# Kernel optimization log

Hardware: AMD Instinct MI355X
Metric: run time of the kernel (lower is better)

The kernel has to match this reference:

```python
import math
import jax, jax.numpy as jnp
import numpy as np
from jax import lax

L = 16
T = 256
FDIM = 3
N_MIN = 4
N_MAX = 64
INIT_RANGE = 1e-4
# low 32 bits of the products are exact in uint32, and XOR + (% T) with T=256
# only reads the low 8 bits, so uint32 arithmetic matches torch's int64 exactly.
PI = jnp.array([1, 2654435761, 805459861], dtype=jnp.uint32)

def _levels():
    growth = math.exp(math.log(N_MAX / N_MIN) / (L - 1))
    return [math.floor(N_MIN * growth ** l) for l in range(L)]

def setup_inputs() -> dict:
    key = jax.random.key(0)
    kx, kt = jax.random.split(key)
    x = jax.random.uniform(kx, (4, 3, 64, 64, 64), dtype=jnp.float32)
    hash_table = (jax.random.uniform(kt, (L, T, FDIM), dtype=jnp.float32) * 2.0
                  - 1.0) * INIT_RANGE
    return {"x": x, "hash_table": hash_table}

def _forward(x, hash_table):
    b, c, h, w, d = x.shape
    outs = []
    for l, n in enumerate(_levels()):
        kh, kw, kd = h // n, w // n, d // n
        # max_pool3d with kernel==stride, VALID padding (torch default)
        pooled = lax.reduce_window(x * n, -jnp.inf, lax.max,
                                   (1, 1, kh, kw, kd), (1, 1, kh, kw, kd),
                                   'VALID')  # [b, 3, nh, nw, nd]
        g = pooled.astype(jnp.uint32)  # trunc toward zero (values >= 0)
        g = g * PI.reshape(1, 3, 1, 1, 1)
        gh = (g[:, 0] ^ g[:, 1] ^ g[:, 2]) % jnp.uint32(T)  # [b, nh, nw, nd]
        feat = hash_table[l][gh]                 # [b, nh, nw, nd, F] gather
        feat = jnp.transpose(feat, (0, 4, 1, 3, 2))  # [b, F, nh, nd, nw]
        up = jax.image.resize(feat, (b, FDIM, h, w, d), method='trilinear')
        outs.append(up)
    return jnp.concatenate(outs, axis=1)  # [b, L*F, h, w, d]

def reference(x, hash_table):
    return _forward(x, hash_table)
```

## Files before the change

kernel.cpp:

```cpp
#include <hip/hip_runtime.h>
#include <cmath>
#include <cstdint>
#include <cstddef>

using u32 = unsigned int;
typedef float f32x4 __attribute__((ext_vector_type(4)));

__device__ inline void st4(float* p, float a, float b, float c, float d)
{
    f32x4 v; v.x = a; v.y = b; v.z = c; v.w = d;
    *(f32x4*)p = v;
}

constexpr int NH[12] = {4,4,5,6,8,10,12,16,21,21,32,32};

constexpr int OFF_M2  = 0;
constexpr int OFF_M3  = 393216;
constexpr int OFF_M5  = 504348;
constexpr int OFF_M4  = 525084;
constexpr int OFF_M6  = 574236;
constexpr int OFF_M8  = 586236;
constexpr int OFF_M10 = 592380;
constexpr int OFF_M12 = 594972;
constexpr int OFF_M16 = 596472;

constexpr int POFF[12] = {OFF_M16,OFF_M16,OFF_M12,OFF_M10,OFF_M8,OFF_M6,
                          OFF_M5, OFF_M4, OFF_M3, OFF_M3, OFF_M2, OFF_M2};

constexpr float invf_of(int nh){ return (float)(1.0/(64.0/(double)nh)); }
constexpr float INVF[12] = {invf_of(4),invf_of(4),invf_of(5),invf_of(6),
                            invf_of(8),invf_of(10),invf_of(12),invf_of(16),
                            invf_of(21),invf_of(21),invf_of(32),invf_of(32)};

struct HP { int n[16]; };

__device__ inline float lp(float a, float b, float w){ return fmaf(w, b - a, a); }

__global__ __launch_bounds__(256) void k_pool_base(const float* __restrict__ x,
                                                   float* __restrict__ ws)
{
    int tid = blockIdx.x * 256 + threadIdx.x;
    if (tid < 393216) {
        int pd = tid & 31, pw = (tid >> 5) & 31, ph = (tid >> 10) & 31;
        int bc = tid >> 15;
        const float* xp = x + (size_t)bc * 262144 + (ph*2)*4096 + (pw*2)*64 + pd*2;
        float2 v00 = *(const float2*)(xp);
        float2 v01 = *(const float2*)(xp + 64);
        float2 v10 = *(const float2*)(xp + 4096);
        float2 v11 = *(const float2*)(xp + 4160);
        float m = fmaxf(fmaxf(fmaxf(v00.x,v00.y), fmaxf(v01.x,v01.y)),
                        fmaxf(fmaxf(v10.x,v10.y), fmaxf(v11.x,v11.y)));
        ws[OFF_M2 + tid] = m;
    } else if (tid < 504348) {
        int idx = tid - 393216;
        int pd = idx % 21; int t2 = idx / 21;
        int pw = t2 % 21;  int t3 = t2 / 21;
        int ph = t3 % 21;  int bc = t3 / 21;
        const float* xp = x + (size_t)bc * 262144 + (ph*3)*4096 + (pw*3)*64 + pd*3;
        float m = -1.f;
        #pragma unroll
        for (int dh = 0; dh < 3; ++dh)
        #pragma unroll
        for (int dw = 0; dw < 3; ++dw) {
            const float* r = xp + dh*4096 + dw*64;
            m = fmaxf(m, fmaxf(fmaxf(r[0], r[1]), r[2]));
        }
        ws[OFF_M3 + idx] = m;
    } else if (tid < 525084) {
        int idx = tid - 504348;
        int pd = idx % 12; int t2 = idx / 12;
        int pw = t2 % 12;  int t3 = t2 / 12;
        int ph = t3 % 12;  int bc = t3 / 12;
        const float* xp = x + (size_t)bc * 262144 + (ph*5)*4096 + (pw*5)*64 + pd*5;
        float m = -1.f;
        #pragma unroll
        for (int dh = 0; dh < 5; ++dh)
        #pragma unroll
        for (int dw = 0; dw < 5; ++dw) {
            const float* r = xp + dh*4096 + dw*64;
            m = fmaxf(m, fmaxf(fmaxf(fmaxf(r[0],r[1]), fmaxf(r[2],r[3])), r[4]));
        }
        ws[OFF_M5 + idx] = m;
    }
}

__global__ __launch_bounds__(256) void k_pyr(float* __restrict__ ws)
{
    int tid = blockIdx.x * 256 + threadIdx.x;
    if (tid < 49152) {
        int w = tid >> 6, lane = tid & 63;
        int pd = w & 3, pw = (w >> 2) & 3, ph = (w >> 4) & 3, bc = w >> 6;
        const float* m2 = ws + OFF_M2 + (size_t)bc*32768 + (ph*8)*1024 + (pw*8)*32 + pd*8;
        float m = -1.f;
        #pragma unroll
        for (int e = 0; e < 8; ++e) {
            int id2 = (e << 6) | lane;
            int dd = id2 & 7, dw = (id2 >> 3) & 7, dh = id2 >> 6;
            m = fmaxf(m, m2[dh*1024 + dw*32 + dd]);
        }
        #pragma unroll
        for (int s = 32; s; s >>= 1) m = fmaxf(m, __shfl_xor(m, s, 64));
        if (lane == 0) ws[OFF_M16 + w] = m;
    } else if (tid < 98304) {
        int idx = tid - 49152;
        int pd = idx & 15, pw = (idx >> 4) & 15, ph = (idx >> 8) & 15, bc = idx >> 12;
        const float* m2 = ws + OFF_M2 + (size_t)bc*32768 + (ph*2)*1024 + (pw*2)*32 + pd*2;
        float2 u0 = *(const float2*)(m2);
        float2 u1 = *(const float2*)(m2 + 32);
        float2 u2 = *(const float2*)(m2 + 1024);
        float2 u3 = *(const float2*)(m2 + 1056);
        ws[OFF_M4 + idx] = fmaxf(fmaxf(fmaxf(u0.x,u0.y), fmaxf(u1.x,u1.y)),
                                 fmaxf(fmaxf(u2.x,u2.y), fmaxf(u3.x,u3.y)));
    } else if (tid < 110304) {
        int idx = tid - 98304;
        int pd = idx % 10; int t2 = idx / 10;
        int pw = t2 % 10;  int t3 = t2 / 10;
        int ph = t3 % 10;  int bc = t3 / 10;
        const float* m2 = ws + OFF_M2 + (size_t)bc*32768 + (ph*3)*1024 + (pw*3)*32 + pd*3;
        float m = -1.f;
        #pragma unroll
        for (int dh = 0; dh < 3; ++dh)
        #pragma unroll
        for (int dw = 0; dw < 3; ++dw) {
            const float* r = m2 + dh*1024 + dw*32;
            m = fmaxf(m, fmaxf(fmaxf(r[0], r[1]), r[2]));
        }
        ws[OFF_M6 + idx] = m;
    } else if (tid < 116448) {
        int idx = tid - 110304;
        int pd = idx & 7, pw = (idx >> 3) & 7, ph = (idx >> 6) & 7, bc = idx >> 9;
        const float* m2 = ws + OFF_M2 + (size_t)bc*32768 + (ph*4)*1024 + (pw*4)*32 + pd*4;
        float m = -1.f;
        #pragma unroll
        for (int dh = 0; dh < 4; ++dh)
        #pragma unroll
        for (int dw = 0; dw < 4; ++dw) {
            float4 v = *(const float4*)(m2 + dh*1024 + dw*32);
            m = fmaxf(m, fmaxf(fmaxf(v.x,v.y), fmaxf(v.z,v.w)));
        }
        ws[OFF_M8 + idx] = m;
    } else if (tid < 119040) {
        int idx = tid - 116448;
        int pd = idx % 6; int t2 = idx / 6;
        int pw = t2 % 6;  int t3 = t2 / 6;
        int ph = t3 % 6;  int bc = t3 / 6;
        const float* m2 = ws + OFF_M2 + (size_t)bc*32768 + (ph*5)*1024 + (pw*5)*32 + pd*5;
        float m = -1.f;
        #pragma unroll
        for (int dh = 0; dh < 5; ++dh)
        #pragma unroll
        for (int dw = 0; dw < 5; ++dw) {
            const float* r = m2 + dh*1024 + dw*32;
            m = fmaxf(m, fmaxf(fmaxf(fmaxf(r[0],r[1]), fmaxf(r[2],r[3])), r[4]));
        }
        ws[OFF_M10 + idx] = m;
    } else if (tid < 120540) {
        int idx = tid - 119040;
        int pd = idx % 5; int t2 = idx / 5;
        int pw = t2 % 5;  int t3 = t2 / 5;
        int ph = t3 % 5;  int bc = t3 / 5;
        const float* m3 = ws + OFF_M3 + (size_t)bc*9261 + (ph*4)*441 + (pw*4)*21 + pd*4;
        float m = -1.f;
        #pragma unroll
        for (int dh = 0; dh < 4; ++dh)
        #pragma unroll
        for (int dw = 0; dw < 4; ++dw) {
            const float* r = m3 + dh*441 + dw*21;
            m = fmaxf(m, fmaxf(fmaxf(r[0],r[1]), fmaxf(r[2],r[3])));
        }
        ws[OFF_M12 + idx] = m;
    }
}

__global__ __launch_bounds__(256) void k_out(const float* __restrict__ x,
                                             const float* __restrict__ ws,
                                             const float* __restrict__ tbl,
                                             float* __restrict__ out, HP hp)
{
    __shared__ float4 shb[3072];
    const int t = threadIdx.x;
    const int l = blockIdx.y;
    const int b = blockIdx.x >> 6, i = blockIdx.x & 63;

    if (l < 12) {
        float4* plane = shb;
        float*  uf    = (float*)(shb + 1056);
        const int nh = NH[l];
        const int pitch = nh + 1;
        const float iv = INVF[l];
        const float nf = (float)hp.n[l];

        float fi = (float)i + 0.5f;
        float pp = fminf(fmaxf(fi * iv - 0.5f, 0.f), (float)(nh - 1));
        int p0 = min((int)pp, nh - 2);
        float wp = pp - (float)p0;

        const int nsq = nh * nh, ncb = nsq * nh;
        const float* M   = ws + POFF[l] + (size_t)b * 3 * ncb;
        const float* Mp0 = M + p0 * nsq;
        const float* Mp1 = Mp0 + nsq;
        const float* tl  = tbl + (size_t)l * 768;

        for (int idx = t; idx < nsq; idx += 256) {
            int w = idx / nh, d = idx - w * nh;
            float a0 = Mp0[idx], a1 = Mp0[idx + ncb], a2 = Mp0[idx + 2*ncb];
            u32 h0 = ((u32)(a0*nf) ^ (((u32)(a1*nf))*2654435761u)
                                   ^ (((u32)(a2*nf))*805459861u)) & 255u;
            const float* t0 = tl + h0 * 3;
            float b0 = Mp1[idx], b1 = Mp1[idx + ncb], b2 = Mp1[idx + 2*ncb];
            u32 h1 = ((u32)(b0*nf) ^ (((u32)(b1*nf))*2654435761u)
                                   ^ (((u32)(b2*nf))*805459861u)) & 255u;
            const float* t1 = tl + h1 * 3;
            plane[d * pitch + w] = make_float4(lp(t0[0], t1[0], wp),
                                               lp(t0[1], t1[1], wp),
                                               lp(t0[2], t1[2], wp), 0.f);
        }
        __syncthreads();

        for (int e = t; e < (nh << 6); e += 256) {
            int r = e >> 6, d = e & 63;
            float fk = (float)d + 0.5f;
            float pq = fminf(fmaxf(fk * iv - 0.5f, 0.f), (float)(nh - 1));
            int q0 = min((int)pq, nh - 2);
            float wq = pq - (float)q0;
            const float4* P = plane + r * pitch;
            float4 A = P[q0], B = P[q0 + 1];
            int ub = r * 204 + d;
            uf[ub]       = lp(A.x, B.x, wq);
            uf[ub + 68]  = lp(A.y, B.y, wq);
            uf[ub + 136] = lp(A.z, B.z, wq);
        }
        __syncthreads();

        float* op = out + (size_t)b * 12582912 + (size_t)(3 * l) * 262144
                        + (size_t)i * 4096;
        #pragma unroll
        for (int it = 0; it < 4; ++it) {
            int pos = it * 256 + t;
            int j = pos >> 4, d0 = (pos & 15) << 2;
            float fj = (float)j + 0.5f;
            float pr = fminf(fmaxf(fj * iv - 0.5f, 0.f), (float)(nh - 1));
            int r0 = min((int)pr, nh - 2);
            float wr = pr - (float)r0;
            const float* u0 = uf + r0 * 204 + d0;
            const float* u1 = u0 + 204;
            f32x4 ax = *(const f32x4*)(u0);
            f32x4 ay = *(const f32x4*)(u0 + 68);
            f32x4 az = *(const f32x4*)(u0 + 136);
            f32x4 bx = *(const f32x4*)(u1);
            f32x4 by = *(const f32x4*)(u1 + 68);
            f32x4 bz = *(const f32x4*)(u1 + 136);
            int off = j * 64 + d0;
            st4(op + off,          lp(ax.x,bx.x,wr), lp(ax.y,bx.y,wr),
                                   lp(ax.z,bx.z,wr), lp(ax.w,bx.w,wr));
            st4(op + off + 262144, lp(ay.x,by.x,wr), lp(ay.y,by.y,wr),
                                   lp(ay.z,by.z,wr), lp(ay.w,by.w,wr));
            st4(op + off + 524288, lp(az.x,bz.x,wr), lp(az.y,bz.y,wr),
                                   lp(az.z,bz.z,wr), lp(az.w,bz.w,wr));
        }
    } else {
        float4* tab = shb;
        float*  xs  = (float*)(shb + 1024);
        const int jh = l - 12;

        for (int v = t; v < 1024; v += 256) {
            const float* te = tbl + (size_t)(3072 + v) * 3;
            tab[v] = make_float4(te[0], te[1], te[2], 0.f);
        }
        const float* xp = x + (size_t)b * 786432 + (size_t)i * 4096 + jh * 32;
        #pragma unroll
        for (int c = 0; c < 3; ++c)
            for (int k = t; k < 2048; k += 256) {
                int w = k >> 5, jl = k & 31;
                xs[c * 2112 + w * 33 + jl] = xp[(size_t)c * 262144 + w * 64 + jl];
            }
        __syncthreads();

        float nfs[4] = {(float)hp.n[12], (float)hp.n[13],
                        (float)hp.n[14], (float)hp.n[15]};
        float* op = out + (size_t)b * 12582912 + (size_t)36 * 262144
                        + (size_t)i * 4096 + jh * 2048;

        #pragma unroll
        for (int it = 0; it < 2; ++it) {
            int pos = it * 256 + t;
            int jl = pos >> 4, d0 = (pos & 15) << 2;
            float xv[3][4];
            #pragma unroll
            for (int dd = 0; dd < 4; ++dd) {
                int wrow = (d0 + dd) * 33 + jl;
                xv[0][dd] = xs[wrow];
                xv[1][dd] = xs[2112 + wrow];
                xv[2][dd] = xs[4224 + wrow];
            }
            #pragma unroll
            for (int u = 0; u < 4; ++u) {
                float4 f[4];
                #pragma unroll
                for (int dd = 0; dd < 4; ++dd) {
                    u32 g0 = (u32)(xv[0][dd] * nfs[u]);
                    u32 g1 = ((u32)(xv[1][dd] * nfs[u])) * 2654435761u;
                    u32 g2 = ((u32)(xv[2][dd] * nfs[u])) * 805459861u;
                    f[dd] = tab[(u << 8) | ((g0 ^ g1 ^ g2) & 255u)];
                }
                int off = u * 786432 + jl * 64 + d0;
                st4(op + off,          f[0].x, f[1].x, f[2].x, f[3].x);
                st4(op + off + 262144, f[0].y, f[1].y, f[2].y, f[3].y);
                st4(op + off + 524288, f[0].z, f[1].z, f[2].z, f[3].z);
            }
        }
    }
}

extern "C" void kernel_launch(void* const* d_in, const int* in_sizes, int n_in,
                              void* d_out, int out_size, void* d_ws, size_t ws_size,
                              hipStream_t stream)
{
    const float* x   = (const float*)d_in[0];
    const float* tbl = (const float*)d_in[1];
    float* out = (float*)d_out;
    float* ws  = (float*)d_ws;

    HP hp;
    double growth = std::exp(std::log(16.0) / 15.0);
    for (int l = 0; l < 16; ++l)
        hp.n[l] = (int)std::floor(4.0 * std::pow(growth, (double)l));

    hipLaunchKernelGGL(k_pool_base, dim3(2052),    dim3(256), 0, stream, x, ws);
    hipLaunchKernelGGL(k_pyr,       dim3(471),     dim3(256), 0, stream, ws);
    hipLaunchKernelGGL(k_out,       dim3(256, 14), dim3(256), 0, stream, x, ws, tbl, out, hp);
}
```

Baseline: 53.36 us.

## Fuse pyramid pooling into single pass from input and flatten output grid

Merges the two pooling kernels into one: coarse levels (4,6,8,10,12,16 cell sizes) are now max-pooled directly from x, with one wavefront per cell and a shuffle reduction, instead of from the intermediate 2x-pooled buffer. This removes one kernel launch and the dependency on the M2 workspace for the coarse levels. In exchange each coarse cell rereads far more of x, relying on cache. The output kernel's 2D grid becomes a 1D grid ordered so the heavy fine-level blocks launch first and the coarse levels follow in descending size, aiming to reduce tail imbalance.

```diff
diff --git a/kernel.cpp b/kernel.cpp
--- a/kernel.cpp
+++ b/kernel.cpp
@@ -36,8 +36,8 @@
 
 __device__ inline float lp(float a, float b, float w){ return fmaf(w, b - a, a); }
 
-__global__ __launch_bounds__(256) void k_pool_base(const float* __restrict__ x,
-                                                   float* __restrict__ ws)
+__global__ __launch_bounds__(256) void k_pool(const float* __restrict__ x,
+                                              float* __restrict__ ws)
 {
     int tid = blockIdx.x * 256 + threadIdx.x;
     if (tid < 393216) {
@@ -81,94 +81,99 @@
             m = fmaxf(m, fmaxf(fmaxf(fmaxf(r[0],r[1]), fmaxf(r[2],r[3])), r[4]));
         }
         ws[OFF_M5 + idx] = m;
-    }
-}
-
-__global__ __launch_bounds__(256) void k_pyr(float* __restrict__ ws)
-{
-    int tid = blockIdx.x * 256 + threadIdx.x;
-    if (tid < 49152) {
-        int w = tid >> 6, lane = tid & 63;
-        int pd = w & 3, pw = (w >> 2) & 3, ph = (w >> 4) & 3, bc = w >> 6;
-        const float* m2 = ws + OFF_M2 + (size_t)bc*32768 + (ph*8)*1024 + (pw*8)*32 + pd*8;
+    } else if (tid < 574236) {
+        int idx = tid - 525084;
+        int pd = idx & 15, pw = (idx >> 4) & 15, ph = (idx >> 8) & 15, bc = idx >> 12;
+        const float* xp = x + (size_t)bc * 262144 + (ph*4)*4096 + (pw*4)*64 + pd*4;
         float m = -1.f;
         #pragma unroll
-        for (int e = 0; e < 8; ++e) {
-            int id2 = (e << 6) | lane;
-            int dd = id2 & 7, dw = (id2 >> 3) & 7, dh = id2 >> 6;
-            m = fmaxf(m, m2[dh*1024 + dw*32 + dd]);
-        }
+        for (int dh = 0; dh < 4; ++dh)
+        #pragma unroll
+        for (int dw = 0; dw < 4; ++dw) {
+            float4 v = *(const float4*)(xp + dh*4096 + dw*64);
+            m = fmaxf(m, fmaxf(fmaxf(v.x,v.y), fmaxf(v.z,v.w)));
+        }
+        ws[OFF_M4 + idx] = m;
+    } else if (tid >= 574464) {
+        int wid  = (tid - 574464) >> 6;
+        int lane = tid & 63;
+        float m = -1.f;
+        const float* xp;
+        int nrounds, kk2, kk, dst;
+        if (wid < 12000) {
+            int c = wid;
+            int pd = c % 10; int t2 = c / 10;
+            int pw = t2 % 10; int t3 = t2 / 10;
+            int ph = t3 % 10; int bc = t3 / 10;
+            xp = x + (size_t)bc * 262144 + (ph*6)*4096 + (pw*6)*64 + pd*6;
+            #pragma unroll
+            for (int r = 0; r < 4; ++r) {
+                int e = lane + (r << 6);
+                if (e < 216) {
+                    int dh = e / 36, rem = e - dh * 36;
+                    int dw = rem / 6, dd = rem - dw * 6;
+                    m = fmaxf(m, xp[dh*4096 + dw*64 + dd]);
+                }
+            }
+            dst = OFF_M6 + wid;
+        } else if (wid < 18144) {
+            int c = wid - 12000;
+            int pd = c & 7, pw = (c >> 3) & 7, ph = (c >> 6) & 7, bc = c >> 9;
+            xp = x + (size_t)bc * 262144 + (ph*8)*4096 + (pw*8)*64 + pd*8;
+            #pragma unroll
+            for (int r = 0; r < 8; ++r) {
+                int e = lane + (r << 6);
+                int dh = e >> 6, dw = (e >> 3) & 7, dd = e & 7;
+                m = fmaxf(m, xp[dh*4096 + dw*64 + dd]);
+            }
+            dst = OFF_M8 + c;
+        } else if (wid < 20736) {
+            int c = wid - 18144;
+            int pd = c % 6; int t2 = c / 6;
+            int pw = t2 % 6; int t3 = t2 / 6;
+            int ph = t3 % 6; int bc = t3 / 6;
+            xp = x + (size_t)bc * 262144 + (ph*10)*4096 + (pw*10)*64 + pd*10;
+            #pragma unroll
+            for (int r = 0; r < 16; ++r) {
+                int e = lane + (r << 6);
+                if (e < 1000) {
+                    int dh = e / 100, rem = e - dh * 100;
+                    int dw = rem / 10, dd = rem - dw * 10;
+                    m = fmaxf(m, xp[dh*4096 + dw*64 + dd]);
+                }
+            }
+            dst = OFF_M10 + c;
+        } else if (wid < 22236) {
+            int c = wid - 20736;
+            int pd = c % 5; int t2 = c / 5;
+            int pw = t2 % 5; int t3 = t2 / 5;
+            int ph = t3 % 5; int bc = t3 / 5;
+            xp = x + (size_t)bc * 262144 + (ph*12)*4096 + (pw*12)*64 + pd*12;
+            #pragma unroll
+            for (int r = 0; r < 27; ++r) {
+                int e = lane + (r << 6);
+                if (e < 1728) {
+                    int dh = e / 144, rem = e - dh * 144;
+                    int dw = rem / 12, dd = rem - dw * 12;
+                    m = fmaxf(m, xp[dh*4096 + dw*64 + dd]);
+                }
+            }
+            dst = OFF_M12 + c;
+        } else if (wid < 23004) {
+            int c = wid - 22236;
+            int pd = c & 3, pw = (c >> 2) & 3, ph = (c >> 4) & 3, bc = c >> 6;
+            xp = x + (size_t)bc * 262144 + (ph*16)*4096 + (pw*16)*64 + pd*16;
+            #pragma unroll
+            for (int r = 0; r < 64; ++r) {
+                int e = lane + (r << 6);
+                int dh = e >> 8, dw = (e >> 4) & 15, dd = e & 15;
+                m = fmaxf(m, xp[dh*4096 + dw*64 + dd]);
+            }
+            dst = OFF_M16 + c;
+        } else return;
         #pragma unroll
         for (int s = 32; s; s >>= 1) m = fmaxf(m, __shfl_xor(m, s, 64));
-        if (lane == 0) ws[OFF_M16 + w] = m;
-    } else if (tid < 98304) {
-        int idx = tid - 49152;
-        int pd = idx & 15, pw = (idx >> 4) & 15, ph = (idx >> 8) & 15, bc = idx >> 12;
-        const float* m2 = ws + OFF_M2 + (size_t)bc*32768 + (ph*2)*1024 + (pw*2)*32 + pd*2;
-        float2 u0 = *(const float2*)(m2);
-        float2 u1 = *(const float2*)(m2 + 32);
-        float2 u2 = *(const float2*)(m2 + 1024);
-        float2 u3 = *(const float2*)(m2 + 1056);
-        ws[OFF_M4 + idx] = fmaxf(fmaxf(fmaxf(u0.x,u0.y), fmaxf(u1.x,u1.y)),
-                                 fmaxf(fmaxf(u2.x,u2.y), fmaxf(u3.x,u3.y)));
-    } else if (tid < 110304) {
-        int idx = tid - 98304;
-        int pd = idx % 10; int t2 = idx / 10;
-        int pw = t2 % 10;  int t3 = t2 / 10;
-        int ph = t3 % 10;  int bc = t3 / 10;
-        const float* m2 = ws + OFF_M2 + (size_t)bc*32768 + (ph*3)*1024 + (pw*3)*32 + pd*3;
-        float m = -1.f;
-        #pragma unroll
-        for (int dh = 0; dh < 3; ++dh)
-        #pragma unroll
-        for (int dw = 0; dw < 3; ++dw) {
-            const float* r = m2 + dh*1024 + dw*32;
-            m = fmaxf(m, fmaxf(fmaxf(r[0], r[1]), r[2]));
-        }
-        ws[OFF_M6 + idx] = m;
-    } else if (tid < 116448) {
-        int idx = tid - 110304;
-        int pd = idx & 7, pw = (idx >> 3) & 7, ph = (idx >> 6) & 7, bc = idx >> 9;
-        const float* m2 = ws + OFF_M2 + (size_t)bc*32768 + (ph*4)*1024 + (pw*4)*32 + pd*4;
-        float m = -1.f;
-        #pragma unroll
-        for (int dh = 0; dh < 4; ++dh)
-        #pragma unroll
-        for (int dw = 0; dw < 4; ++dw) {
-            float4 v = *(const float4*)(m2 + dh*1024 + dw*32);
-            m = fmaxf(m, fmaxf(fmaxf(v.x,v.y), fmaxf(v.z,v.w)));
-        }
-        ws[OFF_M8 + idx] = m;
-    } else if (tid < 119040) {
-        int idx = tid - 116448;
-        int pd = idx % 6; int t2 = idx / 6;
-        int pw = t2 % 6;  int t3 = t2 / 6;
-        int ph = t3 % 6;  int bc = t3 / 6;
-        const float* m2 = ws + OFF_M2 + (size_t)bc*32768 + (ph*5)*1024 + (pw*5)*32 + pd*5;
-        float m = -1.f;
-        #pragma unroll
-        for (int dh = 0; dh < 5; ++dh)
-        #pragma unroll
-        for (int dw = 0; dw < 5; ++dw) {
-            const float* r = m2 + dh*1024 + dw*32;
-            m = fmaxf(m, fmaxf(fmaxf(fmaxf(r[0],r[1]), fmaxf(r[2],r[3])), r[4]));
-        }
-        ws[OFF_M10 + idx] = m;
-    } else if (tid < 120540) {
-        int idx = tid - 119040;
-        int pd = idx % 5; int t2 = idx / 5;
-        int pw = t2 % 5;  int t3 = t2 / 5;
-        int ph = t3 % 5;  int bc = t3 / 5;
-        const float* m3 = ws + OFF_M3 + (size_t)bc*9261 + (ph*4)*441 + (pw*4)*21 + pd*4;
-        float m = -1.f;
-        #pragma unroll
-        for (int dh = 0; dh < 4; ++dh)
-        #pragma unroll
-        for (int dw = 0; dw < 4; ++dw) {
-            const float* r = m3 + dh*441 + dw*21;
-            m = fmaxf(m, fmaxf(fmaxf(r[0],r[1]), fmaxf(r[2],r[3])));
-        }
-        ws[OFF_M12 + idx] = m;
+        if (lane == 0) ws[dst] = m;
     }
 }
 
@@ -179,10 +184,12 @@
 {
     __shared__ float4 shb[3072];
     const int t = threadIdx.x;
-    const int l = blockIdx.y;
-    const int b = blockIdx.x >> 6, i = blockIdx.x & 63;
-
-    if (l < 12) {
+    const int bid = blockIdx.x;
+
+    if (bid >= 512) {
+        const int e = bid - 512;
+        const int l = 11 - (e >> 8);
+        const int b = (e >> 6) & 3, i = e & 63;
         float4* plane = shb;
         float*  uf    = (float*)(shb + 1056);
         const int nh = NH[l];
@@ -217,8 +224,8 @@
         }
         __syncthreads();
 
-        for (int e = t; e < (nh << 6); e += 256) {
-            int r = e >> 6, d = e & 63;
+        for (int e2 = t; e2 < (nh << 6); e2 += 256) {
+            int r = e2 >> 6, d = e2 & 63;
             float fk = (float)d + 0.5f;
             float pq = fminf(fmaxf(fk * iv - 0.5f, 0.f), (float)(nh - 1));
             int q0 = min((int)pq, nh - 2);
@@ -261,7 +268,9 @@
     } else {
         float4* tab = shb;
         float*  xs  = (float*)(shb + 1024);
-        const int jh = l - 12;
+        const int jh = bid & 1;
+        const int i  = (bid >> 1) & 63;
+        const int b  = (bid >> 7) & 3;
 
         for (int v = t; v < 1024; v += 256) {
             const float* te = tbl + (size_t)(3072 + v) * 3;
@@ -326,7 +335,6 @@
     for (int l = 0; l < 16; ++l)
         hp.n[l] = (int)std::floor(4.0 * std::pow(growth, (double)l));
 
-    hipLaunchKernelGGL(k_pool_base, dim3(2052),    dim3(256), 0, stream, x, ws);
-    hipLaunchKernelGGL(k_pyr,       dim3(471),     dim3(256), 0, stream, ws);
-    hipLaunchKernelGGL(k_out,       dim3(256, 14), dim3(256), 0, stream, x, ws, tbl, out, hp);
+    hipLaunchKernelGGL(k_pool, dim3(7995), dim3(256), 0, stream, x, ws);
+    hipLaunchKernelGGL(k_out,  dim3(3584), dim3(256), 0, stream, x, ws, tbl, out, hp);
 }
```

Result: slower. 59.87 us (+12.2%).
